# Kernel tuning notes

Hardware: AMD Instinct MI355X
Metric: run time of the kernel (lower is better)

The kernel has to match this reference:

```python
import jax, jax.numpy as jnp
import numpy as np

B, S, D_IN = 2, 2048, 2048
N_HEADS, N_KV, HEAD_DIM = 16, 4, 128
GROUP = N_HEADS // N_KV  # 4
SCALING = 256.0 ** -0.5  # query_pre_attn_scalar = 256
EPS = 1e-6


def rms_norm(x, scale):
    # RMSNorm over last dim (head_dim)
    var = jnp.mean(jnp.square(x), axis=-1, keepdims=True)
    return x * jax.lax.rsqrt(var + EPS) * scale


def apply_rope(x, cos, sin):
    # x: [b, h, s, d]; cos/sin: [s, d]
    d = x.shape[-1]
    x1, x2 = x[..., : d // 2], x[..., d // 2 :]
    rotated = jnp.concatenate([-x2, x1], axis=-1)
    return x * cos[None, None, :, :] + rotated * sin[None, None, :, :]


def setup_inputs() -> dict:
    key = jax.random.key(0)
    ks = jax.random.split(key, 6)
    x = jax.random.normal(ks[0], (B, S, D_IN), dtype=jnp.float32)
    Wq = jax.random.normal(ks[1], (D_IN, N_HEADS * HEAD_DIM), dtype=jnp.float32) * 0.02
    Wk = jax.random.normal(ks[2], (D_IN, N_KV * HEAD_DIM), dtype=jnp.float32) * 0.02
    Wv = jax.random.normal(ks[3], (D_IN, N_KV * HEAD_DIM), dtype=jnp.float32) * 0.02
    Wo = jax.random.normal(ks[4], (N_HEADS * HEAD_DIM, D_IN), dtype=jnp.float32) * 0.02
    q_scale = jnp.ones((HEAD_DIM,), dtype=jnp.float32)
    k_scale = jnp.ones((HEAD_DIM,), dtype=jnp.float32)
    # RoPE tables: angles repeated twice across head_dim
    inv_freq = 1.0 / (10000.0 ** (np.arange(0, HEAD_DIM, 2, dtype=np.float32) / HEAD_DIM))
    angles = np.arange(S, dtype=np.float32)[:, None] * inv_freq[None, :]  # [S, d/2]
    angles = np.concatenate([angles, angles], axis=-1)  # [S, d]
    cos = jnp.asarray(np.cos(angles), dtype=jnp.float32)
    sin = jnp.asarray(np.sin(angles), dtype=jnp.float32)
    # causal mask: True = masked (future positions)
    mask = jnp.triu(jnp.ones((S, S), dtype=bool), k=1)
    return {"x": x, "mask": mask, "cos": cos, "sin": sin,
            "Wq": Wq, "Wk": Wk, "Wv": Wv, "Wo": Wo,
            "q_scale": q_scale, "k_scale": k_scale}


def reference(x, mask, cos, sin, Wq, Wk, Wv, Wo, q_scale, k_scale):
    b, s, _ = x.shape
    q = (x @ Wq).reshape(b, s, N_HEADS, HEAD_DIM).transpose(0, 2, 1, 3)  # [b,h,s,d]
    k = (x @ Wk).reshape(b, s, N_KV, HEAD_DIM).transpose(0, 2, 1, 3)     # [b,g,s,d]
    v = (x @ Wv).reshape(b, s, N_KV, HEAD_DIM).transpose(0, 2, 1, 3)
    # qk-norm
    q = rms_norm(q, q_scale)
    k = rms_norm(k, k_scale)
    # RoPE
    q = apply_rope(q, cos, sin)
    k = apply_rope(k, cos, sin)
    # repeat KV across groups
    k = jnp.repeat(k, GROUP, axis=1)  # [b,h,s,d]
    v = jnp.repeat(v, GROUP, axis=1)
    q = q * SCALING
    scores = jnp.einsum('bhqd,bhkd->bhqk', q, k)
    scores = jnp.where(mask, -jnp.inf, scores)
    weights = jax.nn.softmax(scores, axis=-1)
    ctx = jnp.einsum('bhqk,bhkd->bhqd', weights, v)
    ctx = ctx.transpose(0, 2, 1, 3).reshape(b, s, N_HEADS * HEAD_DIM)
    return ctx @ Wo
```

## Files before the change

kernel.cpp:

```cpp
#include <hip/hip_runtime.h>
#include <hip/hip_bf16.h>


using u16 = unsigned short;
using u32 = unsigned int;

constexpr int Ss  = 2048;
constexpr int Hh  = 16;
constexpr int KVH = 4;

typedef __attribute__((ext_vector_type(8))) short bf16x8;
typedef __attribute__((ext_vector_type(4))) float f32x4;

__device__ inline float b2f(u16 v)  { return __uint_as_float(((u32)v) << 16); }
__device__ inline u16 f2bf(float x) {
  u32 u = __float_as_uint(x);
  return (u16)((u + 0x7fffu + ((u >> 16) & 1u)) >> 16);
}
__device__ inline u32 cvtpk(float lo, float hi) {
  u32 r;
  asm("v_cvt_pk_bf16_f32 %0, %1, %2" : "=v"(r) : "v"(lo), "v"(hi));
  return r;
}

typedef const __attribute__((address_space(1))) unsigned int gas_u32;
typedef __attribute__((address_space(3))) unsigned int las_u32;
__device__ inline void gl16(const void* g, void* l) {
  __builtin_amdgcn_global_load_lds((gas_u32*)g, (las_u32*)l, 16, 0, 0);
}

__global__ __launch_bounds__(256) void cvt_bf16(const float* __restrict__ in,
                                                u16* __restrict__ out, int n4) {
  int i = blockIdx.x * 256 + threadIdx.x;
  if (i < n4) {
    float4 f = reinterpret_cast<const float4*>(in)[i];
    ushort4 o;
    o.x = f2bf(f.x); o.y = f2bf(f.y); o.z = f2bf(f.z); o.w = f2bf(f.w);
    reinterpret_cast<ushort4*>(out)[i] = o;
  }
}

__global__ __launch_bounds__(256) void tcvt(const float* __restrict__ in,
                                            u16* __restrict__ out, int N, int K) {
  __shared__ u16 T[64][66];
  const int k0 = blockIdx.x * 64, n0 = blockIdx.y * 64;
  const int c = threadIdx.x & 63, rb = threadIdx.x >> 6;
#pragma unroll
  for (int p = 0; p < 16; p++) {
    int r = p * 4 + rb;
    T[c][r] = f2bf(in[(size_t)(k0 + r) * N + n0 + c]);
  }
  __syncthreads();
#pragma unroll
  for (int p = 0; p < 16; p++) {
    int nr = p * 4 + rb;
    out[(size_t)(n0 + nr) * K + k0 + c] = T[nr][c];
  }
}

__global__ __launch_bounds__(256) void vtrans(const u16* __restrict__ kv,
                                              u16* __restrict__ vT) {
  __shared__ u16 T[64][66];
  const int s0 = blockIdx.x * 64, d0 = blockIdx.y * 64, z = blockIdx.z;
  const int b = z >> 2, kvh = z & 3;
  const int c = threadIdx.x & 63, rb = threadIdx.x >> 6;
#pragma unroll
  for (int p = 0; p < 16; p++) {
    int r = p * 4 + rb;
    T[c][r] = kv[(size_t)(b * Ss + s0 + r) * 1024 + 512 + kvh * 128 + d0 + c];
  }
  __syncthreads();
#pragma unroll
  for (int p = 0; p < 16; p++) {
    int dr = p * 4 + rb;
    vT[((size_t)z * 128 + d0 + dr) * Ss + s0 + c] = T[dr][c];
  }
}

template <int MODE>
__global__ __launch_bounds__(256, 2) void gemm128(const u16* __restrict__ A,
                                                  const u16* __restrict__ Bt,
                                                  void* __restrict__ C0,
                                                  u16* __restrict__ C1,
                                                  int K) {
  __shared__ u16 As[2][128 * 64];
  __shared__ u16 Bs[2][128 * 64];
  const int t = threadIdx.x;
  const int wid = t >> 6, lane = t & 63;
  const int lrow = lane & 15, quad = lane >> 4;
  const int wm = wid >> 1, wn = wid & 1;
  const int m0 = blockIdx.x * 128, n0 = blockIdx.y * 128;
  const int sw8 = (lrow & 7) << 3;

  const int srow = t >> 3;
  const int sco  = ((t & 7) ^ (srow & 7)) * 8;

  f32x4 acc[4][4];
#pragma unroll
  for (int i = 0; i < 4; i++)
#pragma unroll
    for (int j = 0; j < 4; j++) acc[i][j] = (f32x4)0.f;

#define STAGE(buf, k0)                                                     \
  {                                                                        \
    _Pragma("unroll") for (int p = 0; p < 4; p++) {                        \
      gl16(A + (size_t)(m0 + p * 32 + srow) * K + (k0) + sco,              \
           (char*)As[buf] + (p * 256 + t) * 16);                           \
      gl16(Bt + (size_t)(n0 + p * 32 + srow) * K + (k0) + sco,             \
           (char*)Bs[buf] + (p * 256 + t) * 16);                           \
    }                                                                      \
  }

  const int nk = K >> 6;
  STAGE(0, 0)
  STAGE(1, 64)
  asm volatile("s_waitcnt vmcnt(8)" ::: "memory");
  __builtin_amdgcn_s_barrier();
  __builtin_amdgcn_sched_barrier(0);

  for (int kt = 0; kt < nk; ++kt) {
    const int buf = kt & 1;
#pragma unroll
    for (int kc = 0; kc < 2; kc++) {
      bf16x8 af[4], bfr[4];
#pragma unroll
      for (int i = 0; i < 4; i++)
        af[i] = *reinterpret_cast<const bf16x8*>(
            &As[buf][(wm * 64 + i * 16 + lrow) * 64 + (((kc * 4 + quad) << 3) ^ sw8)]);
#pragma unroll
      for (int j = 0; j < 4; j++)
        bfr[j] = *reinterpret_cast<const bf16x8*>(
            &Bs[buf][(wn * 64 + j * 16 + lrow) * 64 + (((kc * 4 + quad) << 3) ^ sw8)]);
      __builtin_amdgcn_s_setprio(1);
#pragma unroll
      for (int i = 0; i < 4; i++)
#pragma unroll
        for (int j = 0; j < 4; j++)
          acc[i][j] =
              __builtin_amdgcn_mfma_f32_16x16x32_bf16(af[i], bfr[j], acc[i][j], 0, 0, 0);
      __builtin_amdgcn_s_setprio(0);
    }
    __builtin_amdgcn_sched_barrier(0);
    __builtin_amdgcn_s_barrier();
    __builtin_amdgcn_sched_barrier(0);
    if (kt + 2 < nk) {
      STAGE(buf, (kt + 2) * 64)
    }
    if (kt + 1 < nk) {
      if (kt + 2 < nk) {
        asm volatile("s_waitcnt vmcnt(8)" ::: "memory");
      } else {
        asm volatile("s_waitcnt vmcnt(0)" ::: "memory");
      }
      __builtin_amdgcn_s_barrier();
      __builtin_amdgcn_sched_barrier(0);
    }
  }
#undef STAGE

  if (MODE == 0) {
    u16* C;
    int stride, coff;
    if (n0 < 2048) { C = (u16*)C0; stride = 2048; coff = n0; }
    else           { C = C1;       stride = 1024; coff = n0 - 2048; }
#pragma unroll
    for (int i = 0; i < 4; i++)
#pragma unroll
      for (int j = 0; j < 4; j++)
#pragma unroll
        for (int r = 0; r < 4; r++) {
          int row = m0 + wm * 64 + i * 16 + quad * 4 + r;
          int col = coff + wn * 64 + j * 16 + lrow;
          C[(size_t)row * stride + col] = f2bf(acc[i][j][r]);
        }
  } else {
    float* C = (float*)C0;
#pragma unroll
    for (int i = 0; i < 4; i++)
#pragma unroll
      for (int j = 0; j < 4; j++)
#pragma unroll
        for (int r = 0; r < 4; r++) {
          int row = m0 + wm * 64 + i * 16 + quad * 4 + r;
          int col = n0 + wn * 64 + j * 16 + lrow;
          C[(size_t)row * 2048 + col] = acc[i][j][r];
        }
  }
}

__global__ __launch_bounds__(256) void rmsrope2(u16* __restrict__ qbuf,
                                                u16* __restrict__ kvb,
                                                const float* __restrict__ qsc,
                                                const float* __restrict__ ksc,
                                                const float* __restrict__ cosb,
                                                const float* __restrict__ sinb) {
  const int w = threadIdx.x >> 6, lane = threadIdx.x & 63;
  const int vi = blockIdx.x * 4 + w;
  const int tok = vi / 20, j = vi - tok * 20;
  const int s = tok & (Ss - 1);
  const bool isq = j < 16;
  u16* p = isq ? (qbuf + (size_t)tok * 2048 + j * 128)
               : (kvb + (size_t)tok * 1024 + (j - 16) * 128);
  const float* scale = isq ? qsc : ksc;
  const float mult = isq ? 0.0625f : 1.0f;

  u32* p32 = reinterpret_cast<u32*>(p);
  u32 v = p32[lane];
  float e0 = b2f((u16)(v & 0xffff)), e1 = b2f((u16)(v >> 16));
  float ss = e0 * e0 + e1 * e1;
#pragma unroll
  for (int off = 32; off > 0; off >>= 1) ss += __shfl_xor(ss, off);
  float rr = rsqrtf(ss * (1.0f / 128.0f) + 1e-6f);
  float2 sc = reinterpret_cast<const float2*>(scale)[lane];
  float x0 = e0 * rr * sc.x;
  float x1 = e1 * rr * sc.y;
  float px0 = __shfl_xor(x0, 32);
  float px1 = __shfl_xor(x1, 32);
  float2 c  = reinterpret_cast<const float2*>(cosb + s * 128)[lane];
  float2 sn = reinterpret_cast<const float2*>(sinb + s * 128)[lane];
  float sgn = (lane < 32) ? -1.0f : 1.0f;
  float o0 = (x0 * c.x + sgn * px0 * sn.x) * mult;
  float o1 = (x1 * c.y + sgn * px1 * sn.y) * mult;
  p32[lane] = cvtpk(o0, o1);
}

__global__ __launch_bounds__(128, 2) void attn_mfma(const u16* __restrict__ qb,
                                                    const u16* __restrict__ kv,
                                                    const u16* __restrict__ vT,
                                                    u16* __restrict__ ctx) {
  __shared__ u16 Ks[64 * 128];
  __shared__ u16 Vs[128 * 64];
  __shared__ u16 Ps[2][32 * 40];
  const int i = blockIdx.x;
  const int kq = i >> 8, jj = i & 255, x = jj >> 5, hb = jj & 31;
  const int qtile = (kq == 0) ? 31 - x : (kq == 1) ? x : (kq == 2) ? 23 - x : 8 + x;
  const int h = hb & 15, b = hb >> 4;
  const int t = threadIdx.x, w = t >> 6, lane = t & 63;
  const int lrow = lane & 15, quad = lane >> 4;
  const int kvh = h >> 2;
  const int qw = qtile * 64 + w * 32;

  const u16* kbase = kv + (size_t)b * Ss * 1024 + kvh * 128;
  const u16* vbase = vT + (size_t)(b * KVH + kvh) * 128 * Ss;

  const int kr  = t >> 4;
  const int kco = ((t & 15) ^ (kr & 7)) * 8;
  const int vr  = t >> 3;
  const int vco = ((t & 7) ^ (vr & 7)) * 8;
  const int sw8 = (lrow & 7) << 3;

  bf16x8 qf[2][4];
#pragma unroll
  for (int g = 0; g < 2; g++)
#pragma unroll
    for (int c = 0; c < 4; c++)
      qf[g][c] = *reinterpret_cast<const bf16x8*>(
          qb + ((size_t)(b * Ss + qw + g * 16 + lrow) * Hh + h) * 128 + c * 32 + quad * 8);

  f32x4 o[2][8];
#pragma unroll
  for (int g = 0; g < 2; g++)
#pragma unroll
    for (int n = 0; n < 8; n++) o[g][n] = (f32x4)0.f;
  float mx[2] = {-1e30f, -1e30f}, ls[2] = {0.f, 0.f};

  const int ntile = qtile + 1;
  for (int kt = 0; kt < ntile; kt++) {
    const int kb0 = kt * 64;
    __syncthreads();
#pragma unroll
    for (int p8 = 0; p8 < 8; p8++) {
      gl16(kbase + (size_t)(kb0 + p8 * 8 + kr) * 1024 + kco,
           (char*)Ks + (p8 * 128 + t) * 16);
      gl16(vbase + (size_t)(p8 * 16 + vr) * Ss + kb0 + vco,
           (char*)Vs + (p8 * 128 + t) * 16);
    }
    __syncthreads();

    f32x4 st[2][4];
#pragma unroll
    for (int g = 0; g < 2; g++)
#pragma unroll
      for (int mt = 0; mt < 4; mt++) st[g][mt] = (f32x4)0.f;
#pragma unroll
    for (int c = 0; c < 4; c++) {
      bf16x8 kf[4];
#pragma unroll
      for (int mt = 0; mt < 4; mt++)
        kf[mt] = *reinterpret_cast<const bf16x8*>(
            &Ks[(mt * 16 + lrow) * 128 + ((((c * 4 + quad) << 3)) ^ sw8)]);
      __builtin_amdgcn_s_setprio(1);
#pragma unroll
      for (int mt = 0; mt < 4; mt++)
#pragma unroll
        for (int g = 0; g < 2; g++)
          st[g][mt] =
              __builtin_amdgcn_mfma_f32_16x16x32_bf16(kf[mt], qf[g][c], st[g][mt], 0, 0, 0);
      __builtin_amdgcn_s_setprio(0);
    }
    if (kb0 + 63 > qw) {
#pragma unroll
      for (int g = 0; g < 2; g++) {
        int qg = qw + g * 16 + lrow;
#pragma unroll
        for (int mt = 0; mt < 4; mt++) {
          int kg = kb0 + mt * 16 + quad * 4;
#pragma unroll
          for (int r = 0; r < 4; r++)
            st[g][mt][r] = (kg + r > qg) ? -1e30f : st[g][mt][r];
        }
      }
    }
    float tmv[2];
#pragma unroll
    for (int g = 0; g < 2; g++) {
      f32x4 m4;
#pragma unroll
      for (int r = 0; r < 4; r++)
        m4[r] = fmaxf(fmaxf(st[g][0][r], st[g][1][r]), fmaxf(st[g][2][r], st[g][3][r]));
      float tm = fmaxf(fmaxf(m4[0], m4[1]), fmaxf(m4[2], m4[3]));
      tm = fmaxf(tm, __shfl_xor(tm, 16));
      tm = fmaxf(tm, __shfl_xor(tm, 32));
      tmv[g] = tm;
    }
    if (__any((tmv[0] > mx[0] + 8.0f) || (tmv[1] > mx[1] + 8.0f))) {
#pragma unroll
      for (int g = 0; g < 2; g++) {
        float mn = fmaxf(mx[g], tmv[g]);
        float a = __expf(mx[g] - mn);
        mx[g] = mn;
        ls[g] *= a;
#pragma unroll
        for (int n = 0; n < 8; n++) o[g][n] *= a;
      }
    }
#pragma unroll
    for (int g = 0; g < 2; g++) {
      float tsum = 0.f;
#pragma unroll
      for (int mt = 0; mt < 4; mt++)
#pragma unroll
        for (int r = 0; r < 4; r++) {
          float pv = __expf(st[g][mt][r] - mx[g]);
          st[g][mt][r] = pv;
          tsum += pv;
        }
      tsum += __shfl_xor(tsum, 16);
      tsum += __shfl_xor(tsum, 32);
      ls[g] += tsum;
    }
#pragma unroll
    for (int c2 = 0; c2 < 2; c2++) {
#pragma unroll
      for (int g = 0; g < 2; g++)
#pragma unroll
        for (int mh = 0; mh < 2; mh++) {
          const f32x4 sv = st[g][c2 * 2 + mh];
          uint2 pk;
          pk.x = cvtpk(sv[0], sv[1]);
          pk.y = cvtpk(sv[2], sv[3]);
          *reinterpret_cast<uint2*>(
              &Ps[w][(g * 16 + lrow) * 40 + mh * 16 + quad * 4]) = pk;
        }
      bf16x8 pfr[2];
#pragma unroll
      for (int g = 0; g < 2; g++)
        pfr[g] = *reinterpret_cast<const bf16x8*>(
            &Ps[w][(g * 16 + lrow) * 40 + quad * 8]);
      __builtin_amdgcn_s_setprio(1);
#pragma unroll
      for (int n = 0; n < 8; n++) {
        bf16x8 vf = *reinterpret_cast<const bf16x8*>(
            &Vs[(n * 16 + lrow) * 64 + ((((c2 * 4 + quad) << 3)) ^ sw8)]);
#pragma unroll
        for (int g = 0; g < 2; g++)
          o[g][n] = __builtin_amdgcn_mfma_f32_16x16x32_bf16(vf, pfr[g], o[g][n], 0, 0, 0);
      }
      __builtin_amdgcn_s_setprio(0);
    }
  }

#pragma unroll
  for (int g = 0; g < 2; g++) {
    float linv = 1.0f / ls[g];
    u16* obase = ctx + ((size_t)(b * Ss + qw + g * 16 + lrow) * Hh + h) * 128 + quad * 4;
#pragma unroll
    for (int n = 0; n < 8; n++) {
      uint2 pk;
      pk.x = cvtpk(o[g][n][0] * linv, o[g][n][1] * linv);
      pk.y = cvtpk(o[g][n][2] * linv, o[g][n][3] * linv);
      *reinterpret_cast<uint2*>(obase + n * 16) = pk;
    }
  }
}

extern "C" void kernel_launch(void* const* d_in, const int* in_sizes, int n_in,
                              void* d_out, int out_size, void* d_ws, size_t ws_size,
                              hipStream_t stream) {
  const float* x    = (const float*)d_in[0];
  const float* cosb = (const float*)d_in[2];
  const float* sinb = (const float*)d_in[3];
  const float* Wq   = (const float*)d_in[4];
  const float* Wk   = (const float*)d_in[5];
  const float* Wv   = (const float*)d_in[6];
  const float* Wo   = (const float*)d_in[7];
  const float* qsc  = (const float*)d_in[8];
  const float* ksc  = (const float*)d_in[9];

  const int M = 2 * Ss;
  u16* xb   = (u16*)d_ws;
  u16* Wqkv = xb + (size_t)8388608;
  u16* qbuf = Wqkv + (size_t)6291456;
  u16* kvb  = qbuf + (size_t)8388608;
  u16* vTb  = xb;
  u16* WoT  = Wqkv;

  cvt_bf16<<<8192, 256, 0, stream>>>(x, xb, 2097152);

  tcvt<<<dim3(32, 32), 256, 0, stream>>>(Wq, Wqkv, 2048, 2048);
  tcvt<<<dim3(32, 8), 256, 0, stream>>>(Wk, Wqkv + (size_t)2048 * 2048, 512, 2048);
  tcvt<<<dim3(32, 8), 256, 0, stream>>>(Wv, Wqkv + (size_t)2560 * 2048, 512, 2048);

  gemm128<0><<<dim3(32, 24), 256, 0, stream>>>(xb, Wqkv, qbuf, kvb, 2048);

  rmsrope2<<<(M * 20) / 4, 256, 0, stream>>>(qbuf, kvb, qsc, ksc, cosb, sinb);

  vtrans<<<dim3(32, 2, 8), 256, 0, stream>>>(kvb, vTb);

  attn_mfma<<<dim3(1024), 128, 0, stream>>>(qbuf, kvb, vTb, qbuf );

  tcvt<<<dim3(32, 32), 256, 0, stream>>>(Wo, WoT, 2048, 2048);
  gemm128<1><<<dim3(32, 16), 256, 0, stream>>>(qbuf, WoT, d_out, nullptr, 2048);
}
```

Before: 343.9 us.

## Read K/V fragments directly from global memory in attention, regroup block order

The attention kernel stops staging K and V tiles in shared memory and has each wave load its MFMA fragments straight from global memory, relying on L1/L2 caching. This removes the per-tile barriers and LDS traffic. Block indexing is reordered so the heads sharing a KV head run close together, which should improve cache reuse of K/V. The transpose kernels also write 32-bit pairs instead of 16-bit values. The cost is duplicate global loads across the two waves and exposed global latency inside the inner loop.

```diff
diff --git a/kernel.cpp b/kernel.cpp
--- a/kernel.cpp
+++ b/kernel.cpp
@@ -51,10 +51,12 @@
     T[c][r] = f2bf(in[(size_t)(k0 + r) * N + n0 + c]);
   }
   __syncthreads();
-#pragma unroll
-  for (int p = 0; p < 16; p++) {
-    int nr = p * 4 + rb;
-    out[(size_t)(n0 + nr) * K + k0 + c] = T[nr][c];
+  const int c2 = threadIdx.x & 31, rb2 = threadIdx.x >> 5;
+#pragma unroll
+  for (int p = 0; p < 8; p++) {
+    int nr = p * 8 + rb2;
+    u32 v = *reinterpret_cast<const u32*>(&T[nr][c2 * 2]);
+    *reinterpret_cast<u32*>(out + (size_t)(n0 + nr) * K + k0 + c2 * 2) = v;
   }
 }
 
@@ -70,10 +72,12 @@
     T[c][r] = kv[(size_t)(b * Ss + s0 + r) * 1024 + 512 + kvh * 128 + d0 + c];
   }
   __syncthreads();
-#pragma unroll
-  for (int p = 0; p < 16; p++) {
-    int dr = p * 4 + rb;
-    vT[((size_t)z * 128 + d0 + dr) * Ss + s0 + c] = T[dr][c];
+  const int c2 = threadIdx.x & 31, rb2 = threadIdx.x >> 5;
+#pragma unroll
+  for (int p = 0; p < 8; p++) {
+    int dr = p * 8 + rb2;
+    u32 v = *reinterpret_cast<const u32*>(&T[dr][c2 * 2]);
+    *reinterpret_cast<u32*>(vT + ((size_t)z * 128 + d0 + dr) * Ss + s0 + c2 * 2) = v;
   }
 }
 
@@ -228,26 +232,19 @@
                                                     const u16* __restrict__ kv,
                                                     const u16* __restrict__ vT,
                                                     u16* __restrict__ ctx) {
-  __shared__ u16 Ks[64 * 128];
-  __shared__ u16 Vs[128 * 64];
   __shared__ u16 Ps[2][32 * 40];
   const int i = blockIdx.x;
-  const int kq = i >> 8, jj = i & 255, x = jj >> 5, hb = jj & 31;
-  const int qtile = (kq == 0) ? 31 - x : (kq == 1) ? x : (kq == 2) ? 23 - x : 8 + x;
-  const int h = hb & 15, b = hb >> 4;
+  const int g8 = i & 7, s = i >> 3;
+  const int r = s >> 5, pos = s & 31;
+  const int qtile = (r & 1) ? pos : 31 - pos;
+  const int kvh = g8 & 3, b = g8 >> 2;
+  const int h = kvh * 4 + r;
   const int t = threadIdx.x, w = t >> 6, lane = t & 63;
   const int lrow = lane & 15, quad = lane >> 4;
-  const int kvh = h >> 2;
   const int qw = qtile * 64 + w * 32;
 
   const u16* kbase = kv + (size_t)b * Ss * 1024 + kvh * 128;
   const u16* vbase = vT + (size_t)(b * KVH + kvh) * 128 * Ss;
-
-  const int kr  = t >> 4;
-  const int kco = ((t & 15) ^ (kr & 7)) * 8;
-  const int vr  = t >> 3;
-  const int vco = ((t & 7) ^ (vr & 7)) * 8;
-  const int sw8 = (lrow & 7) << 3;
 
   bf16x8 qf[2][4];
 #pragma unroll
@@ -267,15 +264,6 @@
   const int ntile = qtile + 1;
   for (int kt = 0; kt < ntile; kt++) {
     const int kb0 = kt * 64;
-    __syncthreads();
-#pragma unroll
-    for (int p8 = 0; p8 < 8; p8++) {
-      gl16(kbase + (size_t)(kb0 + p8 * 8 + kr) * 1024 + kco,
-           (char*)Ks + (p8 * 128 + t) * 16);
-      gl16(vbase + (size_t)(p8 * 16 + vr) * Ss + kb0 + vco,
-           (char*)Vs + (p8 * 128 + t) * 16);
-    }
-    __syncthreads();
 
     f32x4 st[2][4];
 #pragma unroll
@@ -288,7 +276,7 @@
 #pragma unroll
       for (int mt = 0; mt < 4; mt++)
         kf[mt] = *reinterpret_cast<const bf16x8*>(
-            &Ks[(mt * 16 + lrow) * 128 + ((((c * 4 + quad) << 3)) ^ sw8)]);
+            kbase + (size_t)(kb0 + mt * 16 + lrow) * 1024 + c * 32 + quad * 8);
       __builtin_amdgcn_s_setprio(1);
 #pragma unroll
       for (int mt = 0; mt < 4; mt++)
@@ -306,8 +294,8 @@
         for (int mt = 0; mt < 4; mt++) {
           int kg = kb0 + mt * 16 + quad * 4;
 #pragma unroll
-          for (int r = 0; r < 4; r++)
-            st[g][mt][r] = (kg + r > qg) ? -1e30f : st[g][mt][r];
+          for (int rr = 0; rr < 4; rr++)
+            st[g][mt][rr] = (kg + rr > qg) ? -1e30f : st[g][mt][rr];
         }
       }
     }
@@ -316,8 +304,8 @@
     for (int g = 0; g < 2; g++) {
       f32x4 m4;
 #pragma unroll
-      for (int r = 0; r < 4; r++)
-        m4[r] = fmaxf(fmaxf(st[g][0][r], st[g][1][r]), fmaxf(st[g][2][r], st[g][3][r]));
+      for (int rr = 0; rr < 4; rr++)
+        m4[rr] = fmaxf(fmaxf(st[g][0][rr], st[g][1][rr]), fmaxf(st[g][2][rr], st[g][3][rr]));
       float tm = fmaxf(fmaxf(m4[0], m4[1]), fmaxf(m4[2], m4[3]));
       tm = fmaxf(tm, __shfl_xor(tm, 16));
       tm = fmaxf(tm, __shfl_xor(tm, 32));
@@ -340,9 +328,9 @@
 #pragma unroll
       for (int mt = 0; mt < 4; mt++)
 #pragma unroll
-        for (int r = 0; r < 4; r++) {
-          float pv = __expf(st[g][mt][r] - mx[g]);
-          st[g][mt][r] = pv;
+        for (int rr = 0; rr < 4; rr++) {
+          float pv = __expf(st[g][mt][rr] - mx[g]);
+          st[g][mt][rr] = pv;
           tsum += pv;
         }
       tsum += __shfl_xor(tsum, 16);
@@ -367,16 +355,24 @@
       for (int g = 0; g < 2; g++)
         pfr[g] = *reinterpret_cast<const bf16x8*>(
             &Ps[w][(g * 16 + lrow) * 40 + quad * 8]);
-      __builtin_amdgcn_s_setprio(1);
-#pragma unroll
-      for (int n = 0; n < 8; n++) {
-        bf16x8 vf = *reinterpret_cast<const bf16x8*>(
-            &Vs[(n * 16 + lrow) * 64 + ((((c2 * 4 + quad) << 3)) ^ sw8)]);
-#pragma unroll
-        for (int g = 0; g < 2; g++)
-          o[g][n] = __builtin_amdgcn_mfma_f32_16x16x32_bf16(vf, pfr[g], o[g][n], 0, 0, 0);
+#pragma unroll
+      for (int half = 0; half < 2; half++) {
+        bf16x8 vf[4];
+#pragma unroll
+        for (int n4 = 0; n4 < 4; n4++) {
+          int n = half * 4 + n4;
+          vf[n4] = *reinterpret_cast<const bf16x8*>(
+              vbase + (size_t)(n * 16 + lrow) * Ss + kb0 + c2 * 32 + quad * 8);
+        }
+        __builtin_amdgcn_s_setprio(1);
+#pragma unroll
+        for (int n4 = 0; n4 < 4; n4++)
+#pragma unroll
+          for (int g = 0; g < 2; g++)
+            o[g][half * 4 + n4] = __builtin_amdgcn_mfma_f32_16x16x32_bf16(
+                vf[n4], pfr[g], o[g][half * 4 + n4], 0, 0, 0);
+        __builtin_amdgcn_s_setprio(0);
       }
-      __builtin_amdgcn_s_setprio(0);
     }
   }
 
```

Result: slower. 391.5 us (+13.8%).
